# Performance work log

Hardware: AMD Instinct MI355X
Metric: run time of the kernel (lower is better)

The kernel has to match this reference:

```python
import jax, jax.numpy as jnp
import numpy as np

EPS = 1e-5
N, F, D = 16384, 1024, 8


def setup_inputs() -> dict:
    key = jax.random.key(0)
    k1, k2, k3, k4 = jax.random.split(key, 4)
    x = jax.random.normal(k1, (N, F), dtype=jnp.float32)
    y = jax.random.randint(k2, (N,), 0, D, dtype=jnp.int64)
    # per-domain affine params (BatchNorm1d weight/bias per domain)
    gamma = 1.0 + 0.1 * jax.random.normal(k3, (D, F), dtype=jnp.float32)
    beta = 0.1 * jax.random.normal(k4, (D, F), dtype=jnp.float32)
    return {"x": x, "y": y, "gamma": gamma, "beta": beta}


def reference(x, y, gamma, beta):
    # Domain-specific batchnorm (training mode): per-domain batch stats,
    # biased variance, affine. Domains with 1 sample pass through x;
    # domains with 0 samples contribute nothing (out stays zero).
    d = gamma.shape[0]
    ones = jnp.ones((x.shape[0],), dtype=x.dtype)
    counts = jax.ops.segment_sum(ones, y, num_segments=d)          # [D]
    s1 = jax.ops.segment_sum(x, y, num_segments=d)                 # [D, F]
    s2 = jax.ops.segment_sum(x * x, y, num_segments=d)             # [D, F]
    cnt = jnp.maximum(counts, 1.0)[:, None]                        # avoid /0
    mean = s1 / cnt                                                # [D, F]
    var = s2 / cnt - mean * mean                                   # biased var
    inv = jax.lax.rsqrt(var + EPS)                                 # [D, F]
    xhat = (x - mean[y]) * inv[y]                                  # [N, F]
    out_bn = gamma[y] * xhat + beta[y]
    c = counts[y][:, None]                                         # [N, 1]
    return jnp.where(c > 1.0, out_bn, jnp.where(c == 1.0, x, jnp.zeros_like(x)))
```

## Files before the change

kernel.cpp:

```cpp
#include <hip/hip_runtime.h>


#define EPSV 1e-5f
constexpr int N = 16384;
constexpr int F = 1024;
constexpr int D = 8;
constexpr int RPB = 64;
constexpr int RG = N / RPB;
constexpr int F2 = F / 2;

__global__ __launch_bounds__(256) void k1_partials(
    const float* __restrict__ x, const int* __restrict__ y,
    float* __restrict__ partials, int* __restrict__ cnt_parts) {
  const int t = threadIdx.x;
  const int rg = blockIdx.x >> 1;
  const int h = blockIdx.x & 1;
  const int row0 = rg * RPB;

  __shared__ int hist[D];
  if (t < D) hist[t] = 0;
  __syncthreads();
  if (h == 0 && t < RPB) atomicAdd(&hist[y[row0 + t]], 1);

  float2 a1[D], a2[D];
#pragma unroll
  for (int k = 0; k < D; ++k) {
    a1[k] = make_float2(0.f, 0.f);
    a2[k] = make_float2(0.f, 0.f);
  }

  const float2* __restrict__ x2 = (const float2*)x;
  const int c = h * 256 + t;

#define ACC(K)                         \
  a1[K].x += v.x;                      \
  a1[K].y += v.y;                      \
  a2[K].x = fmaf(v.x, v.x, a2[K].x);   \
  a2[K].y = fmaf(v.y, v.y, a2[K].y);   \
  break;

  float2 vv[8];
  int dd[8];
#pragma unroll
  for (int j = 0; j < 8; ++j) {
    dd[j] = y[row0 + j];
    vv[j] = x2[(size_t)(row0 + j) * F2 + c];
  }
#pragma unroll
  for (int r = 0; r < RPB; r += 8) {
    float2 nv[8];
    int nd[8];
    if (r + 8 < RPB) {
#pragma unroll
      for (int j = 0; j < 8; ++j) {
        nd[j] = y[row0 + r + 8 + j];
        nv[j] = x2[(size_t)(row0 + r + 8 + j) * F2 + c];
      }
    }
#pragma unroll
    for (int j = 0; j < 8; ++j) {
      float2 v = vv[j];
      switch (dd[j]) {
        case 0: ACC(0)
        case 1: ACC(1)
        case 2: ACC(2)
        case 3: ACC(3)
        case 4: ACC(4)
        case 5: ACC(5)
        case 6: ACC(6)
        case 7: ACC(7)
      }
    }
    if (r + 8 < RPB) {
#pragma unroll
      for (int j = 0; j < 8; ++j) {
        vv[j] = nv[j];
        dd[j] = nd[j];
      }
    }
  }
#undef ACC

  float4* __restrict__ p4 = (float4*)partials;
#pragma unroll
  for (int k = 0; k < D; ++k)
    p4[(size_t)(rg * D + k) * F2 + c] =
        make_float4(a1[k].x, a2[k].x, a1[k].y, a2[k].y);

  __syncthreads();
  if (h == 0 && t < D) cnt_parts[rg * D + t] = hist[t];
}

__global__ __launch_bounds__(256) void k2_stats(
    const float* __restrict__ partials, const int* __restrict__ cnt_parts,
    const float* __restrict__ gamma, const float* __restrict__ beta,
    float* __restrict__ scale, float* __restrict__ shift) {
  const int t = threadIdx.x;
  const int i = t & 15;
  const int ch = t >> 4;
  const int p = blockIdx.x * 16 + i;
  const int d = p >> 10;

  __shared__ int sc[256];
  sc[t] = cnt_parts[t * D + d];

  const float2* __restrict__ pp = (const float2*)partials;
  float s1 = 0.f, s2 = 0.f;
#pragma unroll
  for (int r = 0; r < 16; ++r) {
    const int rg = ch * 16 + r;
    float2 v = pp[(size_t)rg * (D * F) + p];
    s1 += v.x;
    s2 += v.y;
  }

  __shared__ float sf[16][16][2];
  sf[ch][i][0] = s1;
  sf[ch][i][1] = s2;
  __syncthreads();
  for (int s = 128; s > 0; s >>= 1) {
    if (t < s) sc[t] += sc[t + s];
    __syncthreads();
  }

  if (t < 16) {
    float r1 = 0.f, r2 = 0.f;
#pragma unroll
    for (int c = 0; c < 16; ++c) {
      r1 += sf[c][t][0];
      r2 += sf[c][t][1];
    }
    const int pw = blockIdx.x * 16 + t;
    const float c = (float)sc[0];
    const float cc = fmaxf(c, 1.f);
    const float mean = r1 / cc;
    const float var = r2 / cc - mean * mean;
    const float inv = rsqrtf(var + EPSV);
    float scv = gamma[pw] * inv;
    float shv = beta[pw] - mean * scv;
    if (c <= 1.f) {
      scv = (c == 1.f) ? 1.f : 0.f;
      shv = 0.f;
    }
    scale[pw] = scv;
    shift[pw] = shv;
  }
}

__global__ __launch_bounds__(256) void k3_apply(
    const float* __restrict__ x, const int* __restrict__ y,
    const float* __restrict__ scale, const float* __restrict__ shift,
    float* __restrict__ out) {
  const int t = threadIdx.x;
  const int n0 = blockIdx.x * 8;

  int dd[8];
#pragma unroll
  for (int j = 0; j < 8; ++j) dd[j] = y[n0 + j];

  float4 xv[8];
#pragma unroll
  for (int j = 0; j < 8; ++j)
    xv[j] = ((const float4*)x)[(size_t)(n0 + j) * 256 + t];

#pragma unroll
  for (int j = 0; j < 8; ++j) {
    const float4 g = ((const float4*)scale)[dd[j] * 256 + t];
    const float4 b = ((const float4*)shift)[dd[j] * 256 + t];
    float4 o;
    o.x = fmaf(xv[j].x, g.x, b.x);
    o.y = fmaf(xv[j].y, g.y, b.y);
    o.z = fmaf(xv[j].z, g.z, b.z);
    o.w = fmaf(xv[j].w, g.w, b.w);
    ((float4*)out)[(size_t)(n0 + j) * 256 + t] = o;
  }
}

extern "C" void kernel_launch(void* const* d_in, const int* in_sizes, int n_in,
                              void* d_out, int out_size, void* d_ws, size_t ws_size,
                              hipStream_t stream) {
  const float* x = (const float*)d_in[0];
  const int* y = (const int*)d_in[1];
  const float* gamma = (const float*)d_in[2];
  const float* beta = (const float*)d_in[3];
  float* out = (float*)d_out;

  float* partials = (float*)d_ws;
  int* cnt_parts = (int*)(partials + (size_t)RG * D * F * 2);
  float* scale = (float*)(cnt_parts + RG * D);
  float* shift = scale + D * F;

  k1_partials<<<RG * 2, 256, 0, stream>>>(x, y, partials, cnt_parts);
  k2_stats<<<512, 256, 0, stream>>>(partials, cnt_parts, gamma, beta, scale, shift);
  k3_apply<<<N / 8, 256, 0, stream>>>(x, y, scale, shift, out);
}
```

Before: 134.8 us.

## Reduce partials in shared memory over 256-row groups to shrink intermediate traffic

```diff
diff --git a/kernel.cpp b/kernel.cpp
--- a/kernel.cpp
+++ b/kernel.cpp
@@ -5,22 +5,27 @@
 constexpr int N = 16384;
 constexpr int F = 1024;
 constexpr int D = 8;
-constexpr int RPB = 64;
-constexpr int RG = N / RPB;
+constexpr int RPG = 256;
+constexpr int RG = N / RPG;
 constexpr int F2 = F / 2;
+constexpr int CCH = 8;
+constexpr int CW = F2 / CCH;
 
 __global__ __launch_bounds__(256) void k1_partials(
     const float* __restrict__ x, const int* __restrict__ y,
     float* __restrict__ partials, int* __restrict__ cnt_parts) {
   const int t = threadIdx.x;
-  const int rg = blockIdx.x >> 1;
-  const int h = blockIdx.x & 1;
-  const int row0 = rg * RPB;
+  const int rg = blockIdx.x >> 3;
+  const int chunk = blockIdx.x & 7;
+  const int row0 = rg * RPG;
+  const int cl = t & 63;
+  const int sub = t >> 6;
+  const int c = chunk * CW + cl;
 
   __shared__ int hist[D];
   if (t < D) hist[t] = 0;
   __syncthreads();
-  if (h == 0 && t < RPB) atomicAdd(&hist[y[row0 + t]], 1);
+  if (chunk == 0) atomicAdd(&hist[y[row0 + t]], 1);
 
   float2 a1[D], a2[D];
 #pragma unroll
@@ -30,7 +35,7 @@
   }
 
   const float2* __restrict__ x2 = (const float2*)x;
-  const int c = h * 256 + t;
+  const int rbase = row0 + sub * 64;
 
 #define ACC(K)                         \
   a1[K].x += v.x;                      \
@@ -43,18 +48,18 @@
   int dd[8];
 #pragma unroll
   for (int j = 0; j < 8; ++j) {
-    dd[j] = y[row0 + j];
-    vv[j] = x2[(size_t)(row0 + j) * F2 + c];
-  }
-#pragma unroll
-  for (int r = 0; r < RPB; r += 8) {
+    dd[j] = y[rbase + j];
+    vv[j] = x2[(size_t)(rbase + j) * F2 + c];
+  }
+#pragma unroll
+  for (int r = 0; r < 64; r += 8) {
     float2 nv[8];
     int nd[8];
-    if (r + 8 < RPB) {
+    if (r + 8 < 64) {
 #pragma unroll
       for (int j = 0; j < 8; ++j) {
-        nd[j] = y[row0 + r + 8 + j];
-        nv[j] = x2[(size_t)(row0 + r + 8 + j) * F2 + c];
+        nd[j] = y[rbase + r + 8 + j];
+        nv[j] = x2[(size_t)(rbase + r + 8 + j) * F2 + c];
       }
     }
 #pragma unroll
@@ -71,7 +76,7 @@
         case 7: ACC(7)
       }
     }
-    if (r + 8 < RPB) {
+    if (r + 8 < 64) {
 #pragma unroll
       for (int j = 0; j < 8; ++j) {
         vv[j] = nv[j];
@@ -81,14 +86,31 @@
   }
 #undef ACC
 
+  __shared__ float4 red[4][D][CW];
+#pragma unroll
+  for (int k = 0; k < D; ++k)
+    red[sub][k][cl] = make_float4(a1[k].x, a2[k].x, a1[k].y, a2[k].y);
+  __syncthreads();
+
   float4* __restrict__ p4 = (float4*)partials;
 #pragma unroll
-  for (int k = 0; k < D; ++k)
-    p4[(size_t)(rg * D + k) * F2 + c] =
-        make_float4(a1[k].x, a2[k].x, a1[k].y, a2[k].y);
-
-  __syncthreads();
-  if (h == 0 && t < D) cnt_parts[rg * D + t] = hist[t];
+  for (int u = 0; u < 2; ++u) {
+    const int idx = t * 2 + u;
+    const int d = idx >> 6;
+    const int col = idx & 63;
+    const float4 v0 = red[0][d][col];
+    const float4 v1 = red[1][d][col];
+    const float4 v2 = red[2][d][col];
+    const float4 v3 = red[3][d][col];
+    float4 w;
+    w.x = (v0.x + v1.x) + (v2.x + v3.x);
+    w.y = (v0.y + v1.y) + (v2.y + v3.y);
+    w.z = (v0.z + v1.z) + (v2.z + v3.z);
+    w.w = (v0.w + v1.w) + (v2.w + v3.w);
+    p4[(size_t)(rg * D + d) * F2 + chunk * CW + col] = w;
+  }
+
+  if (chunk == 0 && t < D) cnt_parts[rg * D + t] = hist[t];
 }
 
 __global__ __launch_bounds__(256) void k2_stats(
@@ -96,41 +118,41 @@
     const float* __restrict__ gamma, const float* __restrict__ beta,
     float* __restrict__ scale, float* __restrict__ shift) {
   const int t = threadIdx.x;
-  const int i = t & 15;
-  const int ch = t >> 4;
-  const int p = blockIdx.x * 16 + i;
+  const int i = t & 31;
+  const int ch = t >> 5;
+  const int p = blockIdx.x * 32 + i;
   const int d = p >> 10;
 
-  __shared__ int sc[256];
-  sc[t] = cnt_parts[t * D + d];
+  __shared__ int sc[RG];
+  if (t < RG) sc[t] = cnt_parts[t * D + d];
 
   const float2* __restrict__ pp = (const float2*)partials;
   float s1 = 0.f, s2 = 0.f;
 #pragma unroll
-  for (int r = 0; r < 16; ++r) {
-    const int rg = ch * 16 + r;
+  for (int r = 0; r < 8; ++r) {
+    const int rg = ch * 8 + r;
     float2 v = pp[(size_t)rg * (D * F) + p];
     s1 += v.x;
     s2 += v.y;
   }
 
-  __shared__ float sf[16][16][2];
+  __shared__ float sf[8][32][2];
   sf[ch][i][0] = s1;
   sf[ch][i][1] = s2;
   __syncthreads();
-  for (int s = 128; s > 0; s >>= 1) {
+  for (int s = 32; s > 0; s >>= 1) {
     if (t < s) sc[t] += sc[t + s];
     __syncthreads();
   }
 
-  if (t < 16) {
+  if (t < 32) {
     float r1 = 0.f, r2 = 0.f;
 #pragma unroll
-    for (int c = 0; c < 16; ++c) {
+    for (int c = 0; c < 8; ++c) {
       r1 += sf[c][t][0];
       r2 += sf[c][t][1];
     }
-    const int pw = blockIdx.x * 16 + t;
+    const int pw = blockIdx.x * 32 + t;
     const float c = (float)sc[0];
     const float cc = fmaxf(c, 1.f);
     const float mean = r1 / cc;
@@ -190,7 +212,7 @@
   float* scale = (float*)(cnt_parts + RG * D);
   float* shift = scale + D * F;
 
-  k1_partials<<<RG * 2, 256, 0, stream>>>(x, y, partials, cnt_parts);
-  k2_stats<<<512, 256, 0, stream>>>(partials, cnt_parts, gamma, beta, scale, shift);
+  k1_partials<<<RG * CCH, 256, 0, stream>>>(x, y, partials, cnt_parts);
+  k2_stats<<<256, 256, 0, stream>>>(partials, cnt_parts, gamma, beta, scale, shift);
   k3_apply<<<N / 8, 256, 0, stream>>>(x, y, scale, shift, out);
 }
```

Measured after the change: 132.4 us. Within noise of the previous version (-1.8%).
